# Kernel tuning notes

Hardware: AMD Instinct MI355X
Metric: run time of the kernel (lower is better)

Reference implementation:

```python
import jax, jax.numpy as jnp
import numpy as np

IN_F = 512
OUT_F = 512

def setup_inputs() -> dict:
    key = jax.random.key(0)
    k1, k2, k3 = jax.random.split(key, 3)
    x = jax.random.normal(k1, (2, 512, IN_F), dtype=jnp.float32)
    # uniform init: a = sqrt(6 / (2 + out_features))
    a = float(np.sqrt(6.0 / (2.0 + OUT_F)))
    W = jax.random.uniform(k2, (OUT_F, IN_F), dtype=jnp.float32, minval=-a, maxval=a)
    bound = float(1.0 / np.sqrt(IN_F))
    b = jax.random.uniform(k3, (OUT_F,), dtype=jnp.float32, minval=-bound, maxval=bound)
    return {"x": x, "W": W, "b": b}

def reference(x, W, b):
    # MAM fully connected (beta == 0 path): for each (row, out-neuron),
    # C = max_k(x_k * w_ok) + min_k(x_k * w_ok), then add bias.
    xf = x.reshape(-1, x.shape[-1])            # (B, in)
    prod = xf[:, None, :] * W[None, :, :]      # (B, out, in) -- the large intermediate
    C = prod.max(axis=-1) + prod.min(axis=-1)  # (B, out)
    C = C + b[None, :]
    return C.reshape(x.shape[:-1] + (W.shape[0],))
```

## Files before the change

kernel.cpp:

```cpp
#include <hip/hip_runtime.h>
#include <math.h>


#define O_TOTAL 512
#define K_TOTAL 512
#define OBLK 64
#define NWAVE 4
#define RPW 2
#define RPB (NWAVE * RPW)
#define KCH 64
#define NCHUNK (K_TOTAL / KCH)

typedef float f32x2 __attribute__((ext_vector_type(2)));

__device__ __forceinline__ f32x2 pk_mul(f32x2 a, f32x2 b) {
  f32x2 d;
  asm("v_pk_mul_f32 %0, %1, %2" : "=v"(d) : "v"(a), "v"(b));
  return d;
}

__device__ __forceinline__ void stage16(const float* g, float* lds_base, int lane) {
#if __has_builtin(__builtin_amdgcn_global_load_lds)
  (void)lane;
  __builtin_amdgcn_global_load_lds(
      (__attribute__((address_space(1))) unsigned int*)g,
      (__attribute__((address_space(3))) unsigned int*)lds_base, 16, 0, 0);
#else
  *reinterpret_cast<float4*>(lds_base + lane * 4) = *reinterpret_cast<const float4*>(g);
#endif
}

__global__ __launch_bounds__(256, 4)
void mam_fc_kernel(const float* __restrict__ x, const float* __restrict__ W,
                   const float* __restrict__ bias, float* __restrict__ out) {
  __shared__ __align__(16) float Wl[2][OBLK * KCH];
  __shared__ __align__(16) float Xl[2][RPB * KCH];

  const int t = threadIdx.x;
  const int lane = t & 63;
  const int wv = __builtin_amdgcn_readfirstlane(t >> 6);
  const int ob = blockIdx.x & 7;
  const int rg = blockIdx.x >> 3;
  const int o0 = ob * OBLK;
  const int rowBase = rg * RPB;

  const float* srcW[4];
  int dstWoff[4];
#pragma unroll
  for (int p = 0; p < 4; ++p) {
    const int orow = wv * 16 + p * 4 + (lane >> 4);
    const int g = (lane & 15) ^ (orow & 15);
    srcW[p] = W + (size_t)(o0 + orow) * K_TOTAL + g * 4;
    dstWoff[p] = (wv * 16 + p * 4) * KCH;
  }
  const float* srcX = x + (size_t)(rowBase + wv * 4 + (lane >> 4)) * K_TOTAL + (lane & 15) * 4;
  const int dstXoff = wv * 4 * KCH;

  float amax[RPW], amin[RPW];
#pragma unroll
  for (int r = 0; r < RPW; ++r) { amax[r] = -INFINITY; amin[r] = INFINITY; }

  const unsigned baseW = (unsigned)(lane * (KCH * 4) + (lane & 15) * 16);
  const unsigned baseX = (unsigned)((wv * RPW) * (KCH * 4));

#pragma unroll
  for (int p = 0; p < 4; ++p) stage16(srcW[p], &Wl[0][dstWoff[p]], lane);
  if (wv < 2) stage16(srcX, &Xl[0][dstXoff], lane);
  __syncthreads();

#pragma unroll 1
  for (int c = 0; c < NCHUNK; ++c) {
    if (c + 1 < NCHUNK) {
      const int b = (c + 1) & 1;
      const int kOff = (c + 1) * KCH;
#pragma unroll
      for (int p = 0; p < 4; ++p) stage16(srcW[p] + kOff, &Wl[b][dstWoff[p]], lane);
      if (wv < 2) stage16(srcX + kOff, &Xl[b][dstXoff], lane);
    }

    const char* wb = (const char*)&Wl[c & 1][0];
    const char* xb = (const char*)&Xl[c & 1][0];
#pragma unroll
    for (int j = 0; j < KCH / 4; ++j) {
      const float4 w4 = *reinterpret_cast<const float4*>(wb + (baseW ^ (unsigned)(j * 16)));
      const f32x2 wlo = {w4.x, w4.y}, whi = {w4.z, w4.w};
#pragma unroll
      for (int r = 0; r < RPW; ++r) {
        const float4 x4 = *reinterpret_cast<const float4*>(
            xb + baseX + r * (KCH * 4) + j * 16);
        const f32x2 a = pk_mul(f32x2{x4.x, x4.y}, wlo);
        const f32x2 b = pk_mul(f32x2{x4.z, x4.w}, whi);
        amax[r] = fmaxf(fmaxf(fmaxf(fmaxf(amax[r], a.x), a.y), b.x), b.y);
        amin[r] = fminf(fminf(fminf(fminf(amin[r], a.x), a.y), b.x), b.y);
      }
    }
    __syncthreads();
  }

  const float bv = bias[o0 + lane];
#pragma unroll
  for (int r = 0; r < RPW; ++r) {
    out[(size_t)(rowBase + wv * RPW + r) * O_TOTAL + o0 + lane] =
        amax[r] + amin[r] + bv;
  }
}

extern "C" void kernel_launch(void* const* d_in, const int* in_sizes, int n_in,
                              void* d_out, int out_size, void* d_ws, size_t ws_size,
                              hipStream_t stream) {
  const float* x = (const float*)d_in[0];
  const float* W = (const float*)d_in[1];
  const float* b = (const float*)d_in[2];
  float* out = (float*)d_out;

  const int nrows = in_sizes[0] / K_TOTAL;
  const int nblocks = (O_TOTAL / OBLK) * (nrows / RPB);
  mam_fc_kernel<<<dim3(nblocks), dim3(256), 0, stream>>>(x, W, b, out);
}
```

Before: 23.77 us.

## Read x directly from global per wave and cache W chunk in registers

Drops the LDS staging of x. Each wave now reads its own rows of x straight from global memory at wave-uniform addresses, which the compiler may turn into scalar loads. Rows per wave go from 2 to 4, and each 64-wide W chunk is held in 16 float4 registers so it is reused across those rows, with one barrier per chunk moved to the loop top. The aim is to cut LDS traffic and reuse W more per load. In exchange, register pressure rises (launch bounds lowered to 2 blocks), the grid is half as large, and the hand-written packed multiply is replaced by scalar multiplies.

```diff
diff --git a/kernel.cpp b/kernel.cpp
--- a/kernel.cpp
+++ b/kernel.cpp
@@ -6,35 +6,27 @@
 #define K_TOTAL 512
 #define OBLK 64
 #define NWAVE 4
-#define RPW 2
+#define RPW 4
 #define RPB (NWAVE * RPW)
 #define KCH 64
 #define NCHUNK (K_TOTAL / KCH)
+#define NJ (KCH / 4)
 
-typedef float f32x2 __attribute__((ext_vector_type(2)));
-
-__device__ __forceinline__ f32x2 pk_mul(f32x2 a, f32x2 b) {
-  f32x2 d;
-  asm("v_pk_mul_f32 %0, %1, %2" : "=v"(d) : "v"(a), "v"(b));
-  return d;
-}
-
-__device__ __forceinline__ void stage16(const float* g, float* lds_base, int lane) {
+__device__ __forceinline__ void stage16(const float* g, float* lds_base) {
 #if __has_builtin(__builtin_amdgcn_global_load_lds)
-  (void)lane;
   __builtin_amdgcn_global_load_lds(
       (__attribute__((address_space(1))) unsigned int*)g,
       (__attribute__((address_space(3))) unsigned int*)lds_base, 16, 0, 0);
 #else
-  *reinterpret_cast<float4*>(lds_base + lane * 4) = *reinterpret_cast<const float4*>(g);
+  *reinterpret_cast<float4*>(lds_base + (threadIdx.x & 63) * 4) =
+      *reinterpret_cast<const float4*>(g);
 #endif
 }
 
-__global__ __launch_bounds__(256, 4)
+__global__ __launch_bounds__(256, 2)
 void mam_fc_kernel(const float* __restrict__ x, const float* __restrict__ W,
                    const float* __restrict__ bias, float* __restrict__ out) {
   __shared__ __align__(16) float Wl[2][OBLK * KCH];
-  __shared__ __align__(16) float Xl[2][RPB * KCH];
 
   const int t = threadIdx.x;
   const int lane = t & 63;
@@ -42,7 +34,7 @@
   const int ob = blockIdx.x & 7;
   const int rg = blockIdx.x >> 3;
   const int o0 = ob * OBLK;
-  const int rowBase = rg * RPB;
+  const int rowBase = rg * RPB + wv * RPW;
 
   const float* srcW[4];
   int dstWoff[4];
@@ -53,54 +45,55 @@
     srcW[p] = W + (size_t)(o0 + orow) * K_TOTAL + g * 4;
     dstWoff[p] = (wv * 16 + p * 4) * KCH;
   }
-  const float* srcX = x + (size_t)(rowBase + wv * 4 + (lane >> 4)) * K_TOTAL + (lane & 15) * 4;
-  const int dstXoff = wv * 4 * KCH;
+
+  const float* xr = x + (size_t)rowBase * K_TOTAL;
 
   float amax[RPW], amin[RPW];
 #pragma unroll
   for (int r = 0; r < RPW; ++r) { amax[r] = -INFINITY; amin[r] = INFINITY; }
 
   const unsigned baseW = (unsigned)(lane * (KCH * 4) + (lane & 15) * 16);
-  const unsigned baseX = (unsigned)((wv * RPW) * (KCH * 4));
 
 #pragma unroll
-  for (int p = 0; p < 4; ++p) stage16(srcW[p], &Wl[0][dstWoff[p]], lane);
-  if (wv < 2) stage16(srcX, &Xl[0][dstXoff], lane);
-  __syncthreads();
+  for (int p = 0; p < 4; ++p) stage16(srcW[p], &Wl[0][dstWoff[p]]);
 
 #pragma unroll 1
   for (int c = 0; c < NCHUNK; ++c) {
+    __syncthreads();
+
     if (c + 1 < NCHUNK) {
-      const int b = (c + 1) & 1;
       const int kOff = (c + 1) * KCH;
 #pragma unroll
-      for (int p = 0; p < 4; ++p) stage16(srcW[p] + kOff, &Wl[b][dstWoff[p]], lane);
-      if (wv < 2) stage16(srcX + kOff, &Xl[b][dstXoff], lane);
+      for (int p = 0; p < 4; ++p)
+        stage16(srcW[p] + kOff, &Wl[(c + 1) & 1][dstWoff[p]]);
     }
 
     const char* wb = (const char*)&Wl[c & 1][0];
-    const char* xb = (const char*)&Xl[c & 1][0];
+    float4 w[NJ];
 #pragma unroll
-    for (int j = 0; j < KCH / 4; ++j) {
-      const float4 w4 = *reinterpret_cast<const float4*>(wb + (baseW ^ (unsigned)(j * 16)));
-      const f32x2 wlo = {w4.x, w4.y}, whi = {w4.z, w4.w};
+    for (int j = 0; j < NJ; ++j)
+      w[j] = *reinterpret_cast<const float4*>(wb + (baseW ^ (unsigned)(j * 16)));
+
 #pragma unroll
-      for (int r = 0; r < RPW; ++r) {
-        const float4 x4 = *reinterpret_cast<const float4*>(
-            xb + baseX + r * (KCH * 4) + j * 16);
-        const f32x2 a = pk_mul(f32x2{x4.x, x4.y}, wlo);
-        const f32x2 b = pk_mul(f32x2{x4.z, x4.w}, whi);
-        amax[r] = fmaxf(fmaxf(fmaxf(fmaxf(amax[r], a.x), a.y), b.x), b.y);
-        amin[r] = fminf(fminf(fminf(fminf(amin[r], a.x), a.y), b.x), b.y);
+    for (int r = 0; r < RPW; ++r) {
+      const float* xrc = xr + (size_t)r * K_TOTAL + c * KCH;
+#pragma unroll
+      for (int j = 0; j < NJ; ++j) {
+        const float4 xv = *reinterpret_cast<const float4*>(xrc + j * 4);
+        const float p0 = xv.x * w[j].x;
+        const float p1 = xv.y * w[j].y;
+        const float p2 = xv.z * w[j].z;
+        const float p3 = xv.w * w[j].w;
+        amax[r] = fmaxf(fmaxf(fmaxf(fmaxf(amax[r], p0), p1), p2), p3);
+        amin[r] = fminf(fminf(fminf(fminf(amin[r], p0), p1), p2), p3);
       }
     }
-    __syncthreads();
   }
 
   const float bv = bias[o0 + lane];
 #pragma unroll
   for (int r = 0; r < RPW; ++r) {
-    out[(size_t)(rowBase + wv * RPW + r) * O_TOTAL + o0 + lane] =
+    out[(size_t)(rowBase + r) * O_TOTAL + o0 + lane] =
         amax[r] + amin[r] + bv;
   }
 }
```

Measured after the change: 25.17 us. 5.9% more time.
